# Optimization experiments

Hardware: AMD Instinct MI355X
Metric: run time of the kernel (lower is better)

Reference implementation:

```python
import jax, jax.numpy as jnp
import numpy as np

IN_DIMS = [16, 16, 16]
OUT_DIMS = [16, 16, 16]
RANKS = [1, 16, 16, 1]
BATCH = 1024


def setup_inputs() -> dict:
    key = jax.random.key(0)
    ks = jax.random.split(key, 1 + len(IN_DIMS))
    vector = jax.random.normal(ks[0], (BATCH, *IN_DIMS), dtype=jnp.float32)
    inp = {"vector": vector}
    for i in range(len(IN_DIMS)):
        shape = (RANKS[i], OUT_DIMS[i], IN_DIMS[i], RANKS[i + 1])
        scale = 1.0 / float(np.sqrt(RANKS[i] * IN_DIMS[i]))
        inp[f"core{i}"] = jax.random.normal(ks[1 + i], shape, dtype=jnp.float32) * scale
    return inp


def _tt_matvec(vector, cores):
    """y = M @ x where M is the TT/MPO matrix defined by `cores`.

    vector: (B, d_in_1, ..., d_in_d). Returns (B, d_out_1, ..., d_out_d).
    Mirrors TTMatrix.metric_projection exactly (output dims absorbed into batch).
    """
    bs0 = vector.shape[0]
    res = vector[:, None]  # (B, r0=1, d_in_1, ..., d_in_d)
    bs = bs0
    for core in cores:
        r, o, i, k = core.shape
        rem = res.shape[3:]  # remaining un-contracted input dims
        res_t = res.reshape(bs, r, i, -1)  # (bs, r, i, x)
        # contract rank-in and input dim: (r,o,i,k),(b,r,i,x) -> (b,k,o,x)
        new = jnp.einsum('roik,brix->bkox', core, res_t)
        new = jnp.transpose(new, (0, 2, 1, 3)).reshape(bs * o, k, *rem)
        bs = bs * o
        res = new
    res = jnp.squeeze(res, axis=-1)  # last rank is 1
    out_dims = [c.shape[1] for c in cores]
    return res.reshape(bs0, *out_dims)


def reference(vector, core0, core1, core2):
    return _tt_matvec(vector, (core0, core1, core2))
```

## Files before the change

### kernel.cpp

```cpp
#include <hip/hip_runtime.h>
#include <hip/hip_bf16.h>


typedef short bf16x8 __attribute__((ext_vector_type(8)));
typedef float f32x4 __attribute__((ext_vector_type(4)));

#define WS_A1_OFF 0
#define WS_A0_OFF 131072
#define WS_A2_OFF 147456
#define WS_NEEDED 155648

__device__ __forceinline__ unsigned short f2bf(float f) {
    union { float f; unsigned int u; } x; x.f = f;
    unsigned int u = x.u;
    u += 0x7fffu + ((u >> 16) & 1u);
    return (unsigned short)(u >> 16);
}

__device__ __forceinline__ unsigned int pk_bf16(float lo, float hi) {
    __hip_bfloat162 h = __float22bfloat162_rn(make_float2(lo, hi));
    unsigned int r;
    __builtin_memcpy(&r, &h, 4);
    return r;
}

__global__ void tt_repack(const float* __restrict__ c0,
                          const float* __restrict__ c1,
                          const float* __restrict__ c2,
                          unsigned short* __restrict__ ws) {
    int idx = blockIdx.x * 256 + threadIdx.x;
    if (idx < 8192) {
        int o2 = idx >> 9, ks = (idx >> 6) & 7, l = idx & 63;
        int k2 = l & 15;
        unsigned short* dst = ws + ((size_t)(o2 * 8 + ks) * 64 + l) * 8;
        #pragma unroll
        for (int j = 0; j < 8; ++j) {
            int k = ks * 32 + ((l >> 4) * 8) + j;
            dst[j] = f2bf(c1[(k & 15) * 4096 + o2 * 256 + (k >> 4) * 16 + k2]);
        }
    } else if (idx < 9216) {
        int t = idx - 8192;
        int o1 = t >> 6, l = t & 63;
        unsigned short* dst = ws + WS_A0_OFF / 2 + ((size_t)o1 * 64 + l) * 8;
        #pragma unroll
        for (int j = 0; j < 8; ++j) {
            int k = ((l >> 4) * 8) + j;
            float v = (l < 32) ? c0[o1 * 256 + k * 16 + (l & 15)] : 0.f;
            dst[j] = f2bf(v);
        }
    } else if (idx < 9728) {
        int t = idx - 9216;
        int ks = t >> 6, l = t & 63;
        unsigned short* dst = ws + WS_A2_OFF / 2 + ((size_t)ks * 64 + l) * 8;
        #pragma unroll
        for (int j = 0; j < 8; ++j) {
            int k = ks * 32 + ((l >> 4) * 8) + j;
            dst[j] = f2bf(c2[(k & 15) * 256 + (l & 15) * 16 + (k >> 4)]);
        }
    }
}

template <bool PACKED>
__global__ __launch_bounds__(512, 2) void tt_main(
    const float* __restrict__ vg, const float* __restrict__ c0,
    const float* __restrict__ c1, const float* __restrict__ c2,
    const unsigned short* __restrict__ ws, float* __restrict__ outg)
{
    __shared__ unsigned short T1[16384];
    __shared__ unsigned short T2[2][16384];

    const int b   = blockIdx.x;
    const int t   = threadIdx.x;
    const int w   = t >> 6;
    const int l   = t & 63;
    const int l15 = l & 15;
    const int lg  = l >> 4;

    bf16x8 fb0[2];
    {
        const float* vb = vg + (size_t)b * 4096;
        #pragma unroll
        for (int nt = 0; nt < 2; ++nt) {
            bf16x8 f = {0, 0, 0, 0, 0, 0, 0, 0};
            if (l < 32) {
                int i2 = 2 * w + nt;
                const float* p = vb + (lg * 8) * 256 + i2 * 16 + l15;
                #pragma unroll
                for (int j = 0; j < 8; ++j) f[j] = (short)f2bf(p[j * 256]);
            }
            fb0[nt] = f;
        }
    }
    bf16x8 fa2[8];
    if constexpr (PACKED) {
        #pragma unroll
        for (int ks = 0; ks < 8; ++ks)
            fa2[ks] = *(const bf16x8*)(ws + WS_A2_OFF / 2 + ((size_t)ks * 64 + l) * 8);
    } else {
        for (int ks = 0; ks < 8; ++ks) {
            bf16x8 f;
            for (int j = 0; j < 8; ++j) {
                int k = ks * 32 + lg * 8 + j;
                f[j] = (short)f2bf(c2[(k & 15) * 256 + l15 * 16 + (k >> 4)]);
            }
            fa2[ks] = f;
        }
    }

    const unsigned short* a1p = PACKED ? (ws + (size_t)l * 8) : nullptr;

    for (int nc = 0; nc < 4; ++nc) {
        unsigned short* T2c = T2[nc & 1];

        bf16x8 fa1p[16];
        bf16x8 fa0p[4];
        if constexpr (PACKED) {
            #pragma unroll
            for (int ks = 0; ks < 8; ++ks) {
                fa1p[ks]     = *(const bf16x8*)(a1p + ((2 * w + 0) * 8 + ks) * 512);
                fa1p[8 + ks] = *(const bf16x8*)(a1p + ((2 * w + 1) * 8 + ks) * 512);
            }
            #pragma unroll
            for (int mtl = 0; mtl < 4; ++mtl)
                fa0p[mtl] = *(const bf16x8*)(ws + WS_A0_OFF / 2 +
                                             ((size_t)(nc * 4 + mtl) * 64 + l) * 8);
        } else {
            for (int rt = 0; rt < 2; ++rt)
                for (int ks = 0; ks < 8; ++ks) {
                    int o2 = 2 * w + rt;
                    bf16x8 f;
                    for (int j = 0; j < 8; ++j) {
                        int k = ks * 32 + lg * 8 + j;
                        f[j] = (short)f2bf(c1[(k & 15) * 4096 + o2 * 256 + (k >> 4) * 16 + l15]);
                    }
                    fa1p[rt * 8 + ks] = f;
                }
            for (int mtl = 0; mtl < 4; ++mtl) {
                bf16x8 f = {0, 0, 0, 0, 0, 0, 0, 0};
                if (l < 32) {
                    for (int j = 0; j < 8; ++j)
                        f[j] = (short)f2bf(c0[(nc * 4 + mtl) * 256 + (lg * 8 + j) * 16 + l15]);
                }
                fa0p[mtl] = f;
            }
        }

        #pragma unroll
        for (int mtl = 0; mtl < 4; ++mtl) {
            #pragma unroll
            for (int nt = 0; nt < 2; ++nt) {
                f32x4 z = {0.f, 0.f, 0.f, 0.f};
                f32x4 d = __builtin_amdgcn_mfma_f32_16x16x32_bf16(fa0p[mtl], fb0[nt], z, 0, 0, 0);
                const int i2 = 2 * w + nt;
                const int n  = mtl * 16 + l15;
                int byte = (n * 512 + (i2 * 16 + lg * 4) * 2) ^ ((l15 & 7) << 4);
                uint2 wv;
                wv.x = pk_bf16(d[0], d[1]);
                wv.y = pk_bf16(d[2], d[3]);
                *(uint2*)((char*)T1 + byte) = wv;
            }
        }
        __syncthreads();

        {
            f32x4 acc[2][4];
            #pragma unroll
            for (int rt = 0; rt < 2; ++rt)
                #pragma unroll
                for (int nt = 0; nt < 4; ++nt) acc[rt][nt] = (f32x4){0.f, 0.f, 0.f, 0.f};

            #pragma unroll
            for (int ks = 0; ks < 8; ++ks) {
                #pragma unroll
                for (int nt = 0; nt < 4; ++nt) {
                    int byte = ((nt * 16 + l15) * 512 + (ks * 32 + lg * 8) * 2) ^ ((l15 & 7) << 4);
                    bf16x8 fb = *(const bf16x8*)((char*)T1 + byte);
                    acc[0][nt] = __builtin_amdgcn_mfma_f32_16x16x32_bf16(fa1p[ks],     fb, acc[0][nt], 0, 0, 0);
                    acc[1][nt] = __builtin_amdgcn_mfma_f32_16x16x32_bf16(fa1p[8 + ks], fb, acc[1][nt], 0, 0, 0);
                }
            }
            #pragma unroll
            for (int rt = 0; rt < 2; ++rt) {
                const int o2 = 2 * w + rt;
                #pragma unroll
                for (int nt = 0; nt < 4; ++nt) {
                    int byte = ((nt * 16 + o2) * 512 + (l15 * 16 + lg * 4) * 2) ^ ((o2 & 7) << 4);
                    uint2 wv;
                    wv.x = pk_bf16(acc[rt][nt][0], acc[rt][nt][1]);
                    wv.y = pk_bf16(acc[rt][nt][2], acc[rt][nt][3]);
                    *(uint2*)((char*)T2c + byte) = wv;
                }
            }
        }
        __syncthreads();

        if (w < 4) {
            f32x4 a3a = {0.f, 0.f, 0.f, 0.f};
            f32x4 a3b = {0.f, 0.f, 0.f, 0.f};
            #pragma unroll
            for (int ks = 0; ks < 8; ks += 2) {
                int byte0 = ((w * 16 + l15) * 512 + ((ks + 0) * 32 + lg * 8) * 2) ^ ((l15 & 7) << 4);
                int byte1 = ((w * 16 + l15) * 512 + ((ks + 1) * 32 + lg * 8) * 2) ^ ((l15 & 7) << 4);
                bf16x8 fbA = *(const bf16x8*)((char*)T2c + byte0);
                bf16x8 fbB = *(const bf16x8*)((char*)T2c + byte1);
                a3a = __builtin_amdgcn_mfma_f32_16x16x32_bf16(fa2[ks],     fbA, a3a, 0, 0, 0);
                a3b = __builtin_amdgcn_mfma_f32_16x16x32_bf16(fa2[ks + 1], fbB, a3b, 0, 0, 0);
            }
            f32x4 acc3 = a3a + a3b;
            float* ob = outg + (size_t)b * 4096;
            *(f32x4*)(ob + (nc * 4 + w) * 256 + l15 * 16 + lg * 4) = acc3;
        }
    }
}

extern "C" void kernel_launch(void* const* d_in, const int* in_sizes, int n_in,
                              void* d_out, int out_size, void* d_ws, size_t ws_size,
                              hipStream_t stream) {
    const float* vg  = (const float*)d_in[0];
    const float* c0g = (const float*)d_in[1];
    const float* c1g = (const float*)d_in[2];
    const float* c2g = (const float*)d_in[3];
    float* outg = (float*)d_out;

    const int B = in_sizes[0] / 4096;
    const bool packed = (ws_size >= (size_t)WS_NEEDED) && (d_ws != nullptr);

    if (packed) {
        tt_repack<<<dim3(38), dim3(256), 0, stream>>>(c0g, c1g, c2g, (unsigned short*)d_ws);
        tt_main<true><<<dim3(B), dim3(512), 0, stream>>>(
            vg, c0g, c1g, c2g, (const unsigned short*)d_ws, outg);
    } else {
        tt_main<false><<<dim3(B), dim3(512), 0, stream>>>(
            vg, c0g, c1g, c2g, nullptr, outg);
    }
}
```

Baseline: 55.05 us.

## Retile stage-2 MFMA as 4x2 per wave and hoist core1 fragments out of loop

Each wave now owns 4 output-rank tiles by 2 column tiles in the second contraction instead of 2 by 4. This lets the core1 A-fragments (32 bf16x8 registers) be loaded once before the nc loop rather than reloaded every iteration. It also halves the T1 LDS B-fragment reads per wave. Core2 fragments move inside the nc loop and are loaded only by the four waves that use them. This raises register pressure (32 VGPR vectors held across the loop) under a 512x2 launch bound, which risks spills or lower occupancy.

```diff
diff --git a/kernel.cpp b/kernel.cpp
--- a/kernel.cpp
+++ b/kernel.cpp
@@ -75,6 +75,8 @@
     const int l   = t & 63;
     const int l15 = l & 15;
     const int lg  = l >> 4;
+    const int mg  = w >> 1;
+    const int ng  = w & 1;
 
     bf16x8 fb0[2];
     {
@@ -91,50 +93,38 @@
             fb0[nt] = f;
         }
     }
-    bf16x8 fa2[8];
+
+    bf16x8 fa1p[32];
     if constexpr (PACKED) {
-        #pragma unroll
-        for (int ks = 0; ks < 8; ++ks)
-            fa2[ks] = *(const bf16x8*)(ws + WS_A2_OFF / 2 + ((size_t)ks * 64 + l) * 8);
+        const unsigned short* a1p = ws + (size_t)l * 8;
+        #pragma unroll
+        for (int rt = 0; rt < 4; ++rt)
+            #pragma unroll
+            for (int ks = 0; ks < 8; ++ks)
+                fa1p[rt * 8 + ks] = *(const bf16x8*)(a1p + ((size_t)((4 * mg + rt) * 8 + ks)) * 512);
     } else {
-        for (int ks = 0; ks < 8; ++ks) {
-            bf16x8 f;
-            for (int j = 0; j < 8; ++j) {
-                int k = ks * 32 + lg * 8 + j;
-                f[j] = (short)f2bf(c2[(k & 15) * 256 + l15 * 16 + (k >> 4)]);
-            }
-            fa2[ks] = f;
-        }
-    }
-
-    const unsigned short* a1p = PACKED ? (ws + (size_t)l * 8) : nullptr;
+        for (int rt = 0; rt < 4; ++rt)
+            for (int ks = 0; ks < 8; ++ks) {
+                int o2 = 4 * mg + rt;
+                bf16x8 f;
+                for (int j = 0; j < 8; ++j) {
+                    int k = ks * 32 + lg * 8 + j;
+                    f[j] = (short)f2bf(c1[(k & 15) * 4096 + o2 * 256 + (k >> 4) * 16 + l15]);
+                }
+                fa1p[rt * 8 + ks] = f;
+            }
+    }
 
     for (int nc = 0; nc < 4; ++nc) {
         unsigned short* T2c = T2[nc & 1];
 
-        bf16x8 fa1p[16];
         bf16x8 fa0p[4];
         if constexpr (PACKED) {
-            #pragma unroll
-            for (int ks = 0; ks < 8; ++ks) {
-                fa1p[ks]     = *(const bf16x8*)(a1p + ((2 * w + 0) * 8 + ks) * 512);
-                fa1p[8 + ks] = *(const bf16x8*)(a1p + ((2 * w + 1) * 8 + ks) * 512);
-            }
             #pragma unroll
             for (int mtl = 0; mtl < 4; ++mtl)
                 fa0p[mtl] = *(const bf16x8*)(ws + WS_A0_OFF / 2 +
                                              ((size_t)(nc * 4 + mtl) * 64 + l) * 8);
         } else {
-            for (int rt = 0; rt < 2; ++rt)
-                for (int ks = 0; ks < 8; ++ks) {
-                    int o2 = 2 * w + rt;
-                    bf16x8 f;
-                    for (int j = 0; j < 8; ++j) {
-                        int k = ks * 32 + lg * 8 + j;
-                        f[j] = (short)f2bf(c1[(k & 15) * 4096 + o2 * 256 + (k >> 4) * 16 + l15]);
-                    }
-                    fa1p[rt * 8 + ks] = f;
-                }
             for (int mtl = 0; mtl < 4; ++mtl) {
                 bf16x8 f = {0, 0, 0, 0, 0, 0, 0, 0};
                 if (l < 32) {
@@ -163,31 +153,35 @@
         __syncthreads();
 
         {
-            f32x4 acc[2][4];
-            #pragma unroll
-            for (int rt = 0; rt < 2; ++rt)
-                #pragma unroll
-                for (int nt = 0; nt < 4; ++nt) acc[rt][nt] = (f32x4){0.f, 0.f, 0.f, 0.f};
+            f32x4 acc[4][2];
+            #pragma unroll
+            for (int rt = 0; rt < 4; ++rt)
+                #pragma unroll
+                for (int ntl = 0; ntl < 2; ++ntl) acc[rt][ntl] = (f32x4){0.f, 0.f, 0.f, 0.f};
 
             #pragma unroll
             for (int ks = 0; ks < 8; ++ks) {
                 #pragma unroll
-                for (int nt = 0; nt < 4; ++nt) {
+                for (int ntl = 0; ntl < 2; ++ntl) {
+                    const int nt = 2 * ng + ntl;
                     int byte = ((nt * 16 + l15) * 512 + (ks * 32 + lg * 8) * 2) ^ ((l15 & 7) << 4);
                     bf16x8 fb = *(const bf16x8*)((char*)T1 + byte);
-                    acc[0][nt] = __builtin_amdgcn_mfma_f32_16x16x32_bf16(fa1p[ks],     fb, acc[0][nt], 0, 0, 0);
-                    acc[1][nt] = __builtin_amdgcn_mfma_f32_16x16x32_bf16(fa1p[8 + ks], fb, acc[1][nt], 0, 0, 0);
-                }
-            }
-            #pragma unroll
-            for (int rt = 0; rt < 2; ++rt) {
-                const int o2 = 2 * w + rt;
-                #pragma unroll
-                for (int nt = 0; nt < 4; ++nt) {
+                    acc[0][ntl] = __builtin_amdgcn_mfma_f32_16x16x32_bf16(fa1p[0 * 8 + ks], fb, acc[0][ntl], 0, 0, 0);
+                    acc[1][ntl] = __builtin_amdgcn_mfma_f32_16x16x32_bf16(fa1p[1 * 8 + ks], fb, acc[1][ntl], 0, 0, 0);
+                    acc[2][ntl] = __builtin_amdgcn_mfma_f32_16x16x32_bf16(fa1p[2 * 8 + ks], fb, acc[2][ntl], 0, 0, 0);
+                    acc[3][ntl] = __builtin_amdgcn_mfma_f32_16x16x32_bf16(fa1p[3 * 8 + ks], fb, acc[3][ntl], 0, 0, 0);
+                }
+            }
+            #pragma unroll
+            for (int rt = 0; rt < 4; ++rt) {
+                const int o2 = 4 * mg + rt;
+                #pragma unroll
+                for (int ntl = 0; ntl < 2; ++ntl) {
+                    const int nt = 2 * ng + ntl;
                     int byte = ((nt * 16 + o2) * 512 + (l15 * 16 + lg * 4) * 2) ^ ((o2 & 7) << 4);
                     uint2 wv;
-                    wv.x = pk_bf16(acc[rt][nt][0], acc[rt][nt][1]);
-                    wv.y = pk_bf16(acc[rt][nt][2], acc[rt][nt][3]);
+                    wv.x = pk_bf16(acc[rt][ntl][0], acc[rt][ntl][1]);
+                    wv.y = pk_bf16(acc[rt][ntl][2], acc[rt][ntl][3]);
                     *(uint2*)((char*)T2c + byte) = wv;
                 }
             }
@@ -195,6 +189,21 @@
         __syncthreads();
 
         if (w < 4) {
+            bf16x8 fa2[8];
+            if constexpr (PACKED) {
+                #pragma unroll
+                for (int ks = 0; ks < 8; ++ks)
+                    fa2[ks] = *(const bf16x8*)(ws + WS_A2_OFF / 2 + ((size_t)ks * 64 + l) * 8);
+            } else {
+                for (int ks = 0; ks < 8; ++ks) {
+                    bf16x8 f;
+                    for (int j = 0; j < 8; ++j) {
+                        int k = ks * 32 + lg * 8 + j;
+                        f[j] = (short)f2bf(c2[(k & 15) * 256 + l15 * 16 + (k >> 4)]);
+                    }
+                    fa2[ks] = f;
+                }
+            }
             f32x4 a3a = {0.f, 0.f, 0.f, 0.f};
             f32x4 a3b = {0.f, 0.f, 0.f, 0.f};
             #pragma unroll
```

New measurement: 57.49 us. +4.4%, slower.
